# Performance work log

Measured on AMD Instinct MI355X. Metric: run time of the kernel, lower is better.

## Reference

```python
import jax, jax.numpy as jnp
import numpy as np
import math

B, W, D, H, K = 32, 512, 512, 8, 64
DH = D // H

def _rms(x, s, eps=1e-6):
    return x / jnp.sqrt(jnp.mean(x * x, axis=-1, keepdims=True) + eps) * s

def _l2n(x):
    return x / (jnp.linalg.norm(x, axis=-1, keepdims=True) + 1e-6)

def _rope(x, fc):
    b, t, h, d = x.shape
    xc = jax.lax.complex(x[..., 0::2], x[..., 1::2])
    xr = xc * fc
    return jnp.stack([xr.real, xr.imag], axis=-1).reshape(b, t, h, d)

def setup_inputs() -> dict:
    key = jax.random.key(0)
    ks = jax.random.split(key, 24)
    n = lambda i, s: jax.random.normal(ks[i], s, jnp.float32) * 0.02
    return {
        'x': jax.random.normal(ks[0], (B, W, D), jnp.float32),
        'epi_keys': _l2n(jax.random.normal(ks[1], (B, K, D), jnp.float32)),
        'epi_vals': jax.random.normal(ks[2], (B, K, D), jnp.float32),
        'epi_age': jax.random.uniform(ks[3], (B, K), jnp.float32, 0.0, 10.0),
        'epi_strength': jax.random.uniform(ks[4], (B, K), jnp.float32, 0.01, 1.0),
        'pos_idx': jnp.arange(W, dtype=jnp.int32),
        'rms1': jnp.ones((D,), jnp.float32), 'rms_kv': jnp.ones((D,), jnp.float32),
        'rms2': jnp.ones((D,), jnp.float32), 'rms_read': jnp.ones((D,), jnp.float32),
        'Wq': n(5, (D, D)), 'bq': jnp.zeros((D,), jnp.float32),
        'Wk': n(6, (D, D)), 'bk': jnp.zeros((D,), jnp.float32),
        'Wv': n(7, (D, D)), 'bv': jnp.zeros((D,), jnp.float32),
        'Wo': n(8, (D, D)), 'bo': jnp.zeros((D,), jnp.float32),
        'W1': n(9, (D, 8 * D)), 'W2': n(10, (4 * D, D)),
        'Wwk': n(11, (D, D)), 'bwk': jnp.zeros((D,), jnp.float32),
        'Wwv': n(12, (D, D)), 'bwv': jnp.zeros((D,), jnp.float32),
        'Wws': n(13, (D, 1)), 'bws': jnp.zeros((1,), jnp.float32),
        'Wg1': n(14, (D + 2, D)), 'bg1': jnp.zeros((D,), jnp.float32),
        'Wg2': n(15, (D, 1)), 'bg2': jnp.zeros((1,), jnp.float32),
    }

def _cell(x, epi_keys, epi_vals, epi_age, epi_strength, pos_idx,
          rms1, rms_kv, rms2, rms_read, Wq, bq, Wk, bk, Wv, bv, Wo, bo,
          W1, W2, Wwk, bwk, Wwv, bwv, Wws, bws, Wg1, bg1, Wg2, bg2):
    Bc, T, Dc = x.shape
    # RoPE freqs at absolute window positions (slice_freqs_cis)
    freqs = 1.0 / (10000.0 ** (jnp.arange(0, DH, 2, dtype=jnp.float32) / DH))  # (DH/2,)
    ang = pos_idx.astype(jnp.float32)[:, None] * freqs[None, :]               # (T, DH/2)
    fc = jax.lax.complex(jnp.cos(ang), jnp.sin(ang))[None, :, None, :]        # (1,T,1,DH/2)
    # --- windowed causal RoPE attention (TransformerBlock) ---
    nx, nkv = _rms(x, rms1), _rms(x, rms_kv)
    q = _rope((nx @ Wq + bq).reshape(Bc, T, H, DH), fc)
    k = _rope((nkv @ Wk + bk).reshape(Bc, T, H, DH), fc)
    v = (nkv @ Wv + bv).reshape(Bc, T, H, DH)
    att = jnp.einsum('bthd,bshd->bhts', q, k) / math.sqrt(DH)
    causal = jnp.tril(jnp.ones((T, T), bool))
    att = jnp.where(causal[None, None], att, -1e9)
    p = jax.nn.softmax(att, axis=-1)
    o = jnp.einsum('bhts,bshd->bthd', p, v).reshape(Bc, T, Dc)
    h1 = x + (o @ Wo + bo)
    gv = _rms(h1, rms2) @ W1
    g, val = jnp.split(gv, 2, axis=-1)
    h2 = h1 + (jax.nn.silu(g) * val) @ W2                                     # (B,T,D)
    # --- window summary query ---
    q_win = jnp.mean(h2, axis=1)                                              # (B,D)
    # --- EpisodicSlotReader ---
    qn = _l2n(q_win)
    kn = _l2n(epi_keys)
    sim_r = jnp.sum(kn * qn[:, None, :], axis=-1)                             # (B,K)
    logits = sim_r + 0.5 * jnp.log(jnp.clip(epi_strength, 0.001, 1e9)) - 0.02 * epi_age
    logits = logits + ((epi_strength > 0.001).astype(jnp.float32) - 1.0) * 1000.0
    w_read = jax.nn.softmax(logits, axis=-1)
    read = _rms(jnp.sum(w_read[:, :, None] * epi_vals, axis=1), rms_read)     # (B,D)
    # --- write projections ---
    write_key = q_win @ Wwk + bwk
    write_val = q_win @ Wwv + bwv
    ws = jnp.clip(jax.nn.sigmoid(q_win @ Wws + bws), 0.0, 1.0)                # (B,1)
    # --- EpisodicSlotWriter (ST top-1 competitive write) ---
    wk_n = _l2n(write_key)
    sim_w = jnp.sum(kn * wk_n[:, None, :], axis=-1)                           # (B,K)
    soft = jax.nn.softmax(sim_w * 50.0, axis=-1)
    hard = jax.nn.one_hot(jnp.argmax(soft, axis=-1), K, dtype=jnp.float32)
    write_w = jax.lax.stop_gradient(hard - soft) + soft
    eff = write_w * ws * 0.5                                                  # (B,K)
    re = eff[:, :, None]
    keys_new = _l2n((1.0 - re) * epi_keys + re * write_key[:, None, :])
    vals_new = (1.0 - re) * epi_vals + re * write_val[:, None, :]
    age_new = (epi_age + 1.0) * (1.0 - write_w)
    sn = epi_strength * 0.995
    sn = jnp.clip(sn + write_w * ws * (1.0 - sn), 0.001, 1.0)
    best_sim = jnp.max(sim_w, axis=-1)                                        # (B,)
    # --- MemoryRecallGate ---
    novelty = (1.0 - best_sim)[:, None]
    xg = jnp.concatenate([q_win, ws, novelty], axis=-1)                       # (B,D+2)
    gate = jax.nn.sigmoid(jax.nn.silu(xg @ Wg1 + bg1) @ Wg2 + bg2)            # (B,1)
    out = h2 + (gate * read)[:, None, :]
    return out, keys_new, vals_new, age_new, sn, gate

def reference(x, epi_keys, epi_vals, epi_age, epi_strength, pos_idx,
              rms1, rms_kv, rms2, rms_read, Wq, bq, Wk, bk, Wv, bv, Wo, bo,
              W1, W2, Wwk, bwk, Wwv, bwv, Wws, bws, Wg1, bg1, Wg2, bg2):
    return _cell(x, epi_keys, epi_vals, epi_age, epi_strength, pos_idx,
                 rms1, rms_kv, rms2, rms_read, Wq, bq, Wk, bk, Wv, bv, Wo, bo,
                 W1, W2, Wwk, bwk, Wwv, bwv, Wws, bws, Wg1, bg1, Wg2, bg2)
```

## Files before the change

### kernel.cpp

```cpp
#include <hip/hip_runtime.h>


#define DEVI __device__ __forceinline__
typedef unsigned short u16;
typedef unsigned int   u32;
typedef __bf16 v8bf __attribute__((ext_vector_type(8)));
typedef float  v4f  __attribute__((ext_vector_type(4)));

DEVI float bf2f(u16 u) { u32 v = ((u32)u) << 16; return __builtin_bit_cast(float, v); }
DEVI u16 f2bf(float f) {
  u32 x = __builtin_bit_cast(u32, f);
  u32 r = x + 0x7fffu + ((x >> 16) & 1u);
  return (u16)(r >> 16);
}
DEVI uint4 pack8(const float* f) {
  u32 a[4];
#pragma unroll
  for (int i = 0; i < 4; ++i)
    a[i] = (u32)f2bf(f[2*i]) | ((u32)f2bf(f[2*i+1]) << 16);
  uint4 v; v.x = a[0]; v.y = a[1]; v.z = a[2]; v.w = a[3]; return v;
}
DEVI void ld8f(const float* p, float* f) {
  float4 a = *(const float4*)p, b = *(const float4*)(p + 4);
  f[0]=a.x; f[1]=a.y; f[2]=a.z; f[3]=a.w; f[4]=b.x; f[5]=b.y; f[6]=b.z; f[7]=b.w;
}
DEVI void st8f(float* p, const float* f) {
  *(float4*)p       = make_float4(f[0], f[1], f[2], f[3]);
  *(float4*)(p + 4) = make_float4(f[4], f[5], f[6], f[7]);
}
DEVI v8bf ldfrag(const u16* p) { return __builtin_bit_cast(v8bf, *(const uint4*)p); }

DEVI u32 rot1(u32 w, float c, float s) {
  float e = bf2f((u16)(w & 0xffffu)), o = bf2f((u16)(w >> 16));
  float ne = e * c - o * s;
  float no = e * s + o * c;
  return (u32)f2bf(ne) | ((u32)f2bf(no) << 16);
}

DEVI void async16(const u16* g, u16* l) {
  __builtin_amdgcn_global_load_lds(
      (const __attribute__((address_space(1))) void*)g,
      (__attribute__((address_space(3))) void*)l, 16, 0, 0);
}

DEVI float wave_sum64(float v) {
  v += __shfl_xor(v, 1);  v += __shfl_xor(v, 2);  v += __shfl_xor(v, 4);
  v += __shfl_xor(v, 8);  v += __shfl_xor(v, 16); v += __shfl_xor(v, 32);
  return v;
}

__device__ float block_sum256(float v, float* sred) {
  v = wave_sum64(v);
  int w = threadIdx.x >> 6;
  __syncthreads();
  if ((threadIdx.x & 63) == 0) sred[w] = v;
  __syncthreads();
  return sred[0] + sred[1] + sred[2] + sred[3];
}

__global__ __launch_bounds__(256) void prep_k(
    const float* __restrict__ Wq, const float* __restrict__ Wk,
    const float* __restrict__ Wv, const float* __restrict__ Wo,
    const float* __restrict__ W1, const float* __restrict__ W2,
    const float* __restrict__ rms1, const float* __restrict__ rms_kv,
    const float* __restrict__ rms2, u16* __restrict__ WTqkv,
    u16* __restrict__ WTo, u16* __restrict__ WT1, u16* __restrict__ WT2,
    const float* __restrict__ bq, const float* __restrict__ bk,
    const float* __restrict__ bv, float* __restrict__ bias_qkv,
    const int* __restrict__ pos, float* __restrict__ tbl,
    float* __restrict__ qw_g, const float* __restrict__ x,
    u16* __restrict__ nrm) {
  int id = blockIdx.x;
  int tid = threadIdx.x;
  if (id >= 4230) {
    int w = tid >> 6, lane = tid & 63;
    size_t row = (size_t)(id - 4230) * 4 + w;
    float xf[8]; ld8f(x + row * 512 + lane * 8, xf);
    float ss = 0.f;
#pragma unroll
    for (int i = 0; i < 8; ++i) ss += xf[i] * xf[i];
    ss = wave_sum64(ss);
    float inv = rsqrtf(ss * (1.f / 512.f) + 1e-6f);
    float of[8];
#pragma unroll
    for (int i = 0; i < 8; ++i) of[i] = xf[i] * inv;
    *(uint4*)(nrm + row * 512 + lane * 8) = pack8(of);
    return;
  }
  if (id >= 4166) {
    qw_g[(id - 4166) * 256 + tid] = 0.f;
    return;
  }
  if (id >= 4102) {
    int idx = (id - 4102) * 256 + tid;
    int t = idx >> 5, f = idx & 31;
    float freq = exp2f(-0.41524101186f * (float)f);
    float ang = (float)pos[t] * freq;
    float sv, cv;
    sincosf(ang, &sv, &cv);
    tbl[t * 64 + f * 2]     = cv;
    tbl[t * 64 + f * 2 + 1] = sv;
    return;
  }
  if (id >= 4096) {
    int j = (id - 4096) * 256 + tid;
    bias_qkv[j] = j < 512 ? bq[j] : (j < 1024 ? bk[j - 512] : bv[j - 1024]);
    return;
  }
  const float* in; const float* scale; u16* outp; int R, C, bx, by;
  if (id < 256)       { in=Wq; scale=rms1;   outp=WTqkv;            R=512;  C=512;  int l=id;       bx=l&15;  by=l>>4; }
  else if (id < 512)  { in=Wk; scale=rms_kv; outp=WTqkv+512*512;    R=512;  C=512;  int l=id-256;   bx=l&15;  by=l>>4; }
  else if (id < 768)  { in=Wv; scale=rms_kv; outp=WTqkv+1024*512;   R=512;  C=512;  int l=id-512;   bx=l&15;  by=l>>4; }
  else if (id < 1024) { in=Wo; scale=nullptr;outp=WTo;              R=512;  C=512;  int l=id-768;   bx=l&15;  by=l>>4; }
  else if (id < 3072) { in=W1; scale=rms2;   outp=WT1;              R=512;  C=4096; int l=id-1024;  bx=l&127; by=l>>7; }
  else                { in=W2; scale=nullptr;outp=WT2;              R=2048; C=512;  int l=id-3072;  bx=l&15;  by=l>>4; }
  __shared__ u16 t[32][33];
  int c0 = bx * 32, r0 = by * 32;
  int lc = tid & 31, lr = tid >> 5;
  for (int rr = lr; rr < 32; rr += 8) {
    float v = in[(size_t)(r0 + rr) * C + c0 + lc];
    if (scale) v *= scale[r0 + rr];
    t[rr][lc] = f2bf(v);
  }
  __syncthreads();
  for (int rr = lr; rr < 32; rr += 8)
    outp[(size_t)(c0 + rr) * R + r0 + lc] = t[lc][rr];
}

__global__ __launch_bounds__(256) void rms_k(const float* __restrict__ x,
                                             u16* __restrict__ o1) {
  int w = threadIdx.x >> 6, lane = threadIdx.x & 63;
  size_t row = (size_t)blockIdx.x * 4 + w;
  float xf[8]; ld8f(x + row * 512 + lane * 8, xf);
  float ss = 0.f;
#pragma unroll
  for (int i = 0; i < 8; ++i) ss += xf[i] * xf[i];
  ss = wave_sum64(ss);
  float inv = rsqrtf(ss * (1.f / 512.f) + 1e-6f);
  float of[8];
#pragma unroll
  for (int i = 0; i < 8; ++i) of[i] = xf[i] * inv;
  *(uint4*)(o1 + row * 512 + lane * 8) = pack8(of);
}

__global__ __launch_bounds__(256) void gemm128_k(const u16* __restrict__ A,
                                                 const u16* __restrict__ BT,
                                                 const float* __restrict__ bias,
                                                 const float* __restrict__ resf,
                                                 u16* __restrict__ outb,
                                                 float* __restrict__ outf,
                                                 float* __restrict__ colsum,
                                                 int N, int Kd) {
  __shared__ u16 As[128 * 64];
  __shared__ u16 Bs[128 * 64];
  int tid = threadIdx.x;
  int w = tid >> 6, lane = tid & 63;
  int m = lane & 15, quad = lane >> 4;
  int wm = w >> 1, wn = w & 1;
  int bm = blockIdx.x, bn = blockIdx.y;
  v4f acc[4][4] = {};
  const int gswz = ((lane & 7) ^ (lane >> 3)) * 8;
  const u16* Ag = A + (size_t)(bm * 128 + w * 32 + (lane >> 3)) * Kd + gswz;
  const u16* Bg = BT + (size_t)(bn * 128 + w * 32 + (lane >> 3)) * Kd + gswz;
  u16* Al = &As[w * 32 * 64];
  u16* Bl = &Bs[w * 32 * 64];
  const int rsw = (m & 7) * 8;
  for (int k0 = 0; k0 < Kd; k0 += 64) {
#pragma unroll
    for (int it = 0; it < 4; ++it) {
      async16(Ag + (size_t)it * 8 * Kd + k0, Al + it * 8 * 64);
      async16(Bg + (size_t)it * 8 * Kd + k0, Bl + it * 8 * 64);
    }
    __syncthreads();
#pragma unroll
    for (int kk = 0; kk < 2; ++kk) {
      v8bf af[4], bfr[4];
#pragma unroll
      for (int i = 0; i < 4; ++i)
        af[i] = ldfrag(&As[(wm * 64 + i * 16 + m) * 64 +
                           ((kk * 32 + quad * 8) ^ rsw)]);
#pragma unroll
      for (int j = 0; j < 4; ++j)
        bfr[j] = ldfrag(&Bs[(wn * 64 + j * 16 + m) * 64 +
                            ((kk * 32 + quad * 8) ^ rsw)]);
#pragma unroll
      for (int i = 0; i < 4; ++i)
#pragma unroll
        for (int j = 0; j < 4; ++j)
          acc[i][j] = __builtin_amdgcn_mfma_f32_16x16x32_bf16(af[i], bfr[j],
                                                              acc[i][j], 0, 0, 0);
    }
    __syncthreads();
  }
  float csum[4] = {0.f, 0.f, 0.f, 0.f};
#pragma unroll
  for (int i = 0; i < 4; ++i) {
    int grow0 = bm * 128 + wm * 64 + i * 16 + quad * 4;
#pragma unroll
    for (int j = 0; j < 4; ++j) {
      int gcol = bn * 128 + wn * 64 + j * 16 + m;
      float bv = bias ? bias[gcol] : 0.f;
#pragma unroll
      for (int rr = 0; rr < 4; ++rr) {
        size_t idx = (size_t)(grow0 + rr) * N + gcol;
        float v = acc[i][j][rr] + bv;
        if (resf) v += resf[idx];
        if (outb) outb[idx] = f2bf(v);
        else      outf[idx] = v;
        if (colsum) csum[j] += v;
      }
    }
  }
  if (colsum) {
    float* cs = (float*)As;
    __syncthreads();
    if (tid < 128) cs[tid] = 0.f;
    __syncthreads();
    int lc = wn * 64 + m;
#pragma unroll
    for (int j = 0; j < 4; ++j) atomicAdd(&cs[lc + j * 16], csum[j]);
    __syncthreads();
    if (tid < 128) {
      int b = bm >> 2;
      atomicAdd(colsum + (size_t)b * 512 + bn * 128 + tid,
                cs[tid] * (1.f / 512.f));
    }
  }
}

__global__ __launch_bounds__(256) void mlp1_k(const u16* __restrict__ A,
                                              const u16* __restrict__ W1T,
                                              u16* __restrict__ out) {
  __shared__ u16 As[128 * 64];
  __shared__ u16 Bgs[64 * 64];
  __shared__ u16 Bvs[64 * 64];
  const int Kd = 512;
  int tid = threadIdx.x;
  int w = tid >> 6, lane = tid & 63;
  int m = lane & 15, quad = lane >> 4;
  int bm = blockIdx.x, bn = blockIdx.y;
  v4f accg[2][4] = {}, accv[2][4] = {};
  const int gswz = ((lane & 7) ^ (lane >> 3)) * 8;
  const u16* Ag  = A + (size_t)(bm * 128 + w * 32 + (lane >> 3)) * Kd + gswz;
  const u16* Bgp = W1T + (size_t)(bn * 64 + w * 16 + (lane >> 3)) * Kd + gswz;
  const u16* Bvp = W1T + (size_t)(2048 + bn * 64 + w * 16 + (lane >> 3)) * Kd + gswz;
  u16* Al  = &As[w * 32 * 64];
  u16* Bgl = &Bgs[w * 16 * 64];
  u16* Bvl = &Bvs[w * 16 * 64];
  const int rsw = (m & 7) * 8;
  for (int k0 = 0; k0 < Kd; k0 += 64) {
#pragma unroll
    for (int it = 0; it < 4; ++it)
      async16(Ag + (size_t)it * 8 * Kd + k0, Al + it * 8 * 64);
#pragma unroll
    for (int it = 0; it < 2; ++it) {
      async16(Bgp + (size_t)it * 8 * Kd + k0, Bgl + it * 8 * 64);
      async16(Bvp + (size_t)it * 8 * Kd + k0, Bvl + it * 8 * 64);
    }
    __syncthreads();
#pragma unroll
    for (int kk = 0; kk < 2; ++kk) {
      v8bf af[2], bg[4], bv[4];
#pragma unroll
      for (int i = 0; i < 2; ++i)
        af[i] = ldfrag(&As[(w * 32 + i * 16 + m) * 64 +
                           ((kk * 32 + quad * 8) ^ rsw)]);
#pragma unroll
      for (int j = 0; j < 4; ++j) {
        bg[j] = ldfrag(&Bgs[(j * 16 + m) * 64 + ((kk * 32 + quad * 8) ^ rsw)]);
        bv[j] = ldfrag(&Bvs[(j * 16 + m) * 64 + ((kk * 32 + quad * 8) ^ rsw)]);
      }
#pragma unroll
      for (int i = 0; i < 2; ++i)
#pragma unroll
        for (int j = 0; j < 4; ++j) {
          accg[i][j] = __builtin_amdgcn_mfma_f32_16x16x32_bf16(af[i], bg[j],
                                                               accg[i][j], 0, 0, 0);
          accv[i][j] = __builtin_amdgcn_mfma_f32_16x16x32_bf16(af[i], bv[j],
                                                               accv[i][j], 0, 0, 0);
        }
    }
    __syncthreads();
  }
#pragma unroll
  for (int i = 0; i < 2; ++i) {
    int grow0 = bm * 128 + w * 32 + i * 16 + quad * 4;
#pragma unroll
    for (int j = 0; j < 4; ++j) {
      int gcol = bn * 64 + j * 16 + m;
#pragma unroll
      for (int rr = 0; rr < 4; ++rr) {
        float g = accg[i][j][rr];
        float sv = g / (1.f + __expf(-g));
        out[(size_t)(grow0 + rr) * 2048 + gcol] = f2bf(sv * accv[i][j][rr]);
      }
    }
  }
}

__global__ __launch_bounds__(1024) void attn_k(const u16* __restrict__ qkv,
                                               const float* __restrict__ tbl,
                                               u16* __restrict__ og) {
  __shared__ u16 Ks[512 * 64];
  __shared__ u16 Vt[64 * 512];
  __shared__ u16 Ps[16][16 * 40];
  int tid = threadIdx.x;
  int w = tid >> 6, lane = tid & 63;
  int m = lane & 15, quad = lane >> 4;
  int bh = blockIdx.x;
  int b = bh >> 3, h = bh & 7;
  const size_t qbase = (size_t)b * 512 * 1536 + h * 64;
  const size_t obase = (size_t)b * 512 * 512 + h * 64;
  const u16* kbase = qkv + (size_t)b * 512 * 1536 + 512 + h * 64;
  const u16* vbase = kbase + 512;

  {
    int d8 = (tid & 7) * 8;
    for (int s = tid >> 3; s < 512; s += 128) {
      uint4 t4 = *(const uint4*)(kbase + (size_t)s * 1536 + d8);
      const float4* tp = (const float4*)(tbl + s * 64 + d8);
      float4 cs01 = tp[0], cs23 = tp[1];
      t4.x = rot1(t4.x, cs01.x, cs01.y);
      t4.y = rot1(t4.y, cs01.z, cs01.w);
      t4.z = rot1(t4.z, cs23.x, cs23.y);
      t4.w = rot1(t4.w, cs23.z, cs23.w);
      *(uint4*)&Ks[s * 64 + (d8 ^ ((s & 7) * 8))] = t4;
    }
  }
  {
    int d0 = (tid & 7) * 8;
    for (int s = tid >> 3; s < 512; s += 128) {
      uint4 v4 = *(const uint4*)(vbase + (size_t)s * 1536 + d0);
      const u16* vv = (const u16*)&v4;
#pragma unroll
      for (int j = 0; j < 8; ++j) {
        int d = d0 + j;
        Vt[d * 512 + (s ^ ((d & 7) * 8))] = vv[j];
      }
    }
  }
  __syncthreads();

  for (int rep = 0; rep < 2; ++rep) {
    int qt = rep == 0 ? w : 31 - w;
    int tb = qt * 16;
    const u16* qp = qkv + qbase + (size_t)(tb + m) * 1536;
    uint4 q0 = *(const uint4*)(qp + quad * 8);
    uint4 q1 = *(const uint4*)(qp + 32 + quad * 8);
    {
      const float* tq = tbl + (tb + m) * 64;
      float4 a = *(const float4*)(tq + quad * 8);
      float4 b4 = *(const float4*)(tq + quad * 8 + 4);
      q0.x = rot1(q0.x, a.x, a.y);   q0.y = rot1(q0.y, a.z, a.w);
      q0.z = rot1(q0.z, b4.x, b4.y); q0.w = rot1(q0.w, b4.z, b4.w);
      float4 c4 = *(const float4*)(tq + 32 + quad * 8);
      float4 d4 = *(const float4*)(tq + 36 + quad * 8);
      q1.x = rot1(q1.x, c4.x, c4.y); q1.y = rot1(q1.y, c4.z, c4.w);
      q1.z = rot1(q1.z, d4.x, d4.y); q1.w = rot1(q1.w, d4.z, d4.w);
    }
    v8bf aq0 = __builtin_bit_cast(v8bf, q0);
    v8bf aq1 = __builtin_bit_cast(v8bf, q1);
    v4f acc[4] = {};
    float mr[4], lr_[4];
#pragma unroll
    for (int rr = 0; rr < 4; ++rr) { mr[rr] = -1.0e30f; lr_[rr] = 0.f; }
    int swz = (m & 7) * 8;

    for (int st2 = 0; st2 <= qt; st2 += 2) {
      int srA = st2 * 16 + m;
      v8bf ka0 = ldfrag(&Ks[srA * 64 + ((quad * 8) ^ swz)]);
      v8bf ka1 = ldfrag(&Ks[srA * 64 + ((32 + quad * 8) ^ swz)]);
      v4f s4a = {};
      __builtin_amdgcn_s_setprio(1);
      s4a = __builtin_amdgcn_mfma_f32_16x16x32_bf16(aq0, ka0, s4a, 0, 0, 0);
      s4a = __builtin_amdgcn_mfma_f32_16x16x32_bf16(aq1, ka1, s4a, 0, 0, 0);
      __builtin_amdgcn_s_setprio(0);
      bool haveB = (st2 + 1 <= qt);
      v4f s4b = {};
      if (haveB) {
        int srB = srA + 16;
        v8bf kb0 = ldfrag(&Ks[srB * 64 + ((quad * 8) ^ swz)]);
        v8bf kb1 = ldfrag(&Ks[srB * 64 + ((32 + quad * 8) ^ swz)]);
        __builtin_amdgcn_s_setprio(1);
        s4b = __builtin_amdgcn_mfma_f32_16x16x32_bf16(aq0, kb0, s4b, 0, 0, 0);
        s4b = __builtin_amdgcn_mfma_f32_16x16x32_bf16(aq1, kb1, s4b, 0, 0, 0);
        __builtin_amdgcn_s_setprio(0);
      }
      float sca[4], scb[4];
#pragma unroll
      for (int rr = 0; rr < 4; ++rr) {
        int rowt = tb + quad * 4 + rr;
        sca[rr] = s4a[rr] * 0.125f;
        if (st2 == qt && st2 * 16 + m > rowt) sca[rr] = -1.0e9f;
        scb[rr] = haveB ? s4b[rr] * 0.125f : -1.0e30f;
        if (haveB && st2 + 1 == qt && (st2 + 1) * 16 + m > rowt) scb[rr] = -1.0e9f;
      }
      float pva[4], pvb[4], alpha[4];
#pragma unroll
      for (int rr = 0; rr < 4; ++rr) {
        float v = fmaxf(sca[rr], scb[rr]);
        v = fmaxf(v, __shfl_xor(v, 1));
        v = fmaxf(v, __shfl_xor(v, 2));
        v = fmaxf(v, __shfl_xor(v, 4));
        v = fmaxf(v, __shfl_xor(v, 8));
        float mn = fmaxf(mr[rr], v);
        alpha[rr] = __expf(mr[rr] - mn);
        pva[rr] = __expf(sca[rr] - mn);
        pvb[rr] = __expf(scb[rr] - mn);
        mr[rr] = mn;
      }
#pragma unroll
      for (int rr = 0; rr < 4; ++rr) {
        float s = pva[rr] + pvb[rr];
        s += __shfl_xor(s, 1); s += __shfl_xor(s, 2);
        s += __shfl_xor(s, 4); s += __shfl_xor(s, 8);
        lr_[rr] = lr_[rr] * alpha[rr] + s;
#pragma unroll
        for (int c = 0; c < 4; ++c) acc[c][rr] *= alpha[rr];
        Ps[w][(quad * 4 + rr) * 40 + m]      = f2bf(pva[rr]);
        Ps[w][(quad * 4 + rr) * 40 + 16 + m] = f2bf(pvb[rr]);
      }
      __asm__ volatile("" ::: "memory");
      v8bf pf = ldfrag(&Ps[w][m * 40 + quad * 8]);
      __builtin_amdgcn_s_setprio(1);
#pragma unroll
      for (int c = 0; c < 4; ++c) {
        int drow = c * 16 + m;
        v8bf vf = ldfrag(&Vt[drow * 512 +
                             ((st2 * 16 + quad * 8) ^ ((drow & 7) * 8))]);
        acc[c] = __builtin_amdgcn_mfma_f32_16x16x32_bf16(pf, vf, acc[c], 0, 0, 0);
      }
      __builtin_amdgcn_s_setprio(0);
    }
#pragma unroll
    for (int rr = 0; rr < 4; ++rr) {
      int t = tb + quad * 4 + rr;
      float inv = 1.f / lr_[rr];
      u16* op = og + obase + (size_t)t * 512;
#pragma unroll
      for (int c = 0; c < 4; ++c) op[c * 16 + m] = f2bf(acc[c][rr] * inv);
    }
  }
}

__global__ __launch_bounds__(256) void gemv_k(
    const float* __restrict__ qw_g, const float* __restrict__ Wwk,
    const float* __restrict__ bwk, const float* __restrict__ Wwv,
    const float* __restrict__ bwv, const float* __restrict__ Wg1,
    const float* __restrict__ bg1, const float* __restrict__ Wws,
    const float* __restrict__ bws, float* __restrict__ wkey_g,
    float* __restrict__ wval_g, float* __restrict__ abase_g,
    float* __restrict__ ws_g) {
  __shared__ float qs[512];
  __shared__ float prt[4][64];
  __shared__ float sred[8];
  int tid = threadIdx.x;
  int b = blockIdx.y, cg = blockIdx.x;
  qs[tid]       = qw_g[(size_t)b * 512 + tid];
  qs[tid + 256] = qw_g[(size_t)b * 512 + tid + 256];
  __syncthreads();
  if (cg == 24) {
    float p = qs[tid] * Wws[tid] + qs[tid + 256] * Wws[tid + 256];
    float tot = block_sum256(p, sred);
    if (tid == 0) {
      float wsv = 1.f / (1.f + __expf(-(tot + bws[0])));
      ws_g[b] = fminf(fmaxf(wsv, 0.f), 1.f);
    }
    return;
  }
  int sel = cg >> 3;
  int c0 = (cg & 7) * 64;
  const float* W = sel == 0 ? Wwk : (sel == 1 ? Wwv : Wg1);
  const float* bias = sel == 0 ? bwk : (sel == 1 ? bwv : bg1);
  float* dst = sel == 0 ? wkey_g : (sel == 1 ? wval_g : abase_g);
  int kg = tid >> 6, cl = tid & 63;
  const float* Wp = W + (size_t)(kg * 128) * 512 + c0 + cl;
  float acc = 0.f;
#pragma unroll 8
  for (int i = 0; i < 128; ++i) acc += qs[kg * 128 + i] * Wp[(size_t)i * 512];
  prt[kg][cl] = acc;
  __syncthreads();
  if (tid < 64)
    dst[(size_t)b * 512 + c0 + tid] =
        prt[0][tid] + prt[1][tid] + prt[2][tid] + prt[3][tid] + bias[c0 + tid];
}

__global__ __launch_bounds__(256) void epi2_k(
    const float* __restrict__ qw_g, const float* __restrict__ wkey_g,
    const float* __restrict__ wval_g, const float* __restrict__ abase_g,
    const float* __restrict__ ws_g, const float* __restrict__ keys,
    const float* __restrict__ vals, const float* __restrict__ age,
    const float* __restrict__ strength, const float* __restrict__ Wg1,
    const float* __restrict__ Wg2, const float* __restrict__ bg2,
    const float* __restrict__ rms_read, float* __restrict__ read_f,
    float* __restrict__ gate_f, float* __restrict__ keys_out,
    float* __restrict__ vals_out, float* __restrict__ age_out,
    float* __restrict__ sn_out, float* __restrict__ gate_out) {
  int b = blockIdx.x;
  int tid = threadIdx.x;
  int w = tid >> 6, lane = tid & 63;
  __shared__ float qs[512], wkl[512], wvl[512];
  __shared__ float knorm[64], sr[64], swv[64], wread[64];
  __shared__ float sred[8];
  __shared__ float scal[2];
  __shared__ int bestk;
  __shared__ float novs;

  qs[tid]        = qw_g[(size_t)b * 512 + tid];
  qs[tid + 256]  = qw_g[(size_t)b * 512 + tid + 256];
  wkl[tid]       = wkey_g[(size_t)b * 512 + tid];
  wkl[tid + 256] = wkey_g[(size_t)b * 512 + tid + 256];
  wvl[tid]       = wval_g[(size_t)b * 512 + tid];
  wvl[tid + 256] = wval_g[(size_t)b * 512 + tid + 256];
  __syncthreads();
  float ws_s = ws_g[b];
  float p = qs[tid] * qs[tid] + qs[tid + 256] * qs[tid + 256];
  float tot = block_sum256(p, sred);
  if (tid == 0) scal[0] = 1.f / (sqrtf(tot) + 1e-6f);
  p = wkl[tid] * wkl[tid] + wkl[tid + 256] * wkl[tid + 256];
  tot = block_sum256(p, sred);
  if (tid == 0) scal[1] = 1.f / (sqrtf(tot) + 1e-6f);
  __syncthreads();
  float qscale = scal[0], wscale = scal[1];
  for (int k = w; k < 64; k += 4) {
    float kf[8];
    ld8f(keys + ((size_t)b * 64 + k) * 512 + lane * 8, kf);
    float s2 = 0.f, sq = 0.f, sw = 0.f;
#pragma unroll
    for (int i = 0; i < 8; ++i) {
      s2 += kf[i] * kf[i];
      sq += kf[i] * qs[lane * 8 + i];
      sw += kf[i] * wkl[lane * 8 + i];
    }
    s2 = wave_sum64(s2);
    sq = wave_sum64(sq);
    sw = wave_sum64(sw);
    if (lane == 0) {
      float kn = sqrtf(s2) + 1e-6f;
      knorm[k] = kn;
      float st = strength[b * 64 + k];
      float ag = age[b * 64 + k];
      sr[k] = (sq * qscale) / kn + 0.5f * logf(fminf(fmaxf(st, 0.001f), 1e9f)) -
              0.02f * ag + ((st > 0.001f) ? 0.f : -1000.f);
      swv[k] = (sw * wscale) / kn;
    }
  }
  __syncthreads();
  if (w == 0) {
    float v = sr[lane];
    float mx = v;
    mx = fmaxf(mx, __shfl_xor(mx, 1));  mx = fmaxf(mx, __shfl_xor(mx, 2));
    mx = fmaxf(mx, __shfl_xor(mx, 4));  mx = fmaxf(mx, __shfl_xor(mx, 8));
    mx = fmaxf(mx, __shfl_xor(mx, 16)); mx = fmaxf(mx, __shfl_xor(mx, 32));
    float e = __expf(v - mx);
    float sm = wave_sum64(e);
    wread[lane] = e / sm;
  } else if (w == 1) {
    float v = swv[lane];
    int idx = lane;
#pragma unroll
    for (int mm = 1; mm < 64; mm <<= 1) {
      float ov = __shfl_xor(v, mm);
      int oi = __shfl_xor(idx, mm);
      if (ov > v || (ov == v && oi < idx)) { v = ov; idx = oi; }
    }
    if (lane == 0) { bestk = idx; novs = 1.f - v; }
  }
  __syncthreads();
  float rv0 = 0.f, rv1 = 0.f;
  for (int k = 0; k < 64; ++k) {
    float wr = wread[k];
    const float* vp = vals + ((size_t)b * 64 + k) * 512;
    rv0 += wr * vp[tid];
    rv1 += wr * vp[tid + 256];
  }
  p = rv0 * rv0 + rv1 * rv1;
  tot = block_sum256(p, sred);
  float rinv = rsqrtf(tot * (1.f / 512.f) + 1e-6f);
  read_f[(size_t)b * 512 + tid]       = rv0 * rinv * rms_read[tid];
  read_f[(size_t)b * 512 + tid + 256] = rv1 * rinv * rms_read[tid + 256];
  if (tid < 64) {
    int k = tid;
    float hard = (k == bestk) ? 1.f : 0.f;
    float ag = age[b * 64 + k];
    age_out[b * 64 + k] = (ag + 1.f) * (1.f - hard);
    float st = strength[b * 64 + k];
    float s0 = st * 0.995f;
    float snv = s0 + hard * ws_s * (1.f - s0);
    sn_out[b * 64 + k] = fminf(fmaxf(snv, 0.001f), 1.f);
  }
  for (int k = w; k < 64; k += 4) {
    float re = (k == bestk) ? ws_s * 0.5f : 0.f;
    float kf[8], vf[8];
    ld8f(keys + ((size_t)b * 64 + k) * 512 + lane * 8, kf);
    ld8f(vals + ((size_t)b * 64 + k) * 512 + lane * 8, vf);
    float u[8], ss = 0.f;
#pragma unroll
    for (int i = 0; i < 8; ++i) {
      u[i] = (1.f - re) * kf[i] + re * wkl[lane * 8 + i];
      ss += u[i] * u[i];
    }
    ss = wave_sum64(ss);
    float uinv = 1.f / (sqrtf(ss) + 1e-6f);
    float ko[8], vo[8];
#pragma unroll
    for (int i = 0; i < 8; ++i) {
      ko[i] = u[i] * uinv;
      vo[i] = (1.f - re) * vf[i] + re * wvl[lane * 8 + i];
    }
    st8f(keys_out + ((size_t)b * 64 + k) * 512 + lane * 8, ko);
    st8f(vals_out + ((size_t)b * 64 + k) * 512 + lane * 8, vo);
  }
  __syncthreads();
  float nov = novs;
  float a0 = abase_g[(size_t)b * 512 + tid] +
             ws_s * Wg1[(size_t)512 * 512 + tid] +
             nov * Wg1[(size_t)513 * 512 + tid];
  float a1 = abase_g[(size_t)b * 512 + tid + 256] +
             ws_s * Wg1[(size_t)512 * 512 + tid + 256] +
             nov * Wg1[(size_t)513 * 512 + tid + 256];
  float h0 = a0 / (1.f + __expf(-a0));
  float h1v = a1 / (1.f + __expf(-a1));
  float gp = h0 * Wg2[tid] + h1v * Wg2[tid + 256];
  tot = block_sum256(gp, sred);
  if (tid == 0) {
    float g = 1.f / (1.f + __expf(-(tot + bg2[0])));
    gate_f[b] = g;
    gate_out[b] = g;
  }
}

__global__ __launch_bounds__(256) void final_k(const float* __restrict__ h2,
                                               const float* __restrict__ read_f,
                                               const float* __restrict__ gate_f,
                                               float* __restrict__ outp) {
  size_t i2 = ((size_t)blockIdx.x * 256 + threadIdx.x) * 2;
  int b = (int)(i2 >> 18);
  int d = (int)(i2 & 511);
  float g = gate_f[b];
  float2 h = *(const float2*)(h2 + i2);
  outp[i2]     = h.x + g * read_f[b * 512 + d];
  outp[i2 + 1] = h.y + g * read_f[b * 512 + d + 1];
}

extern "C" void kernel_launch(void* const* d_in, const int* in_sizes, int n_in,
                              void* d_out, int out_size, void* d_ws,
                              size_t ws_size, hipStream_t stream) {
  const float* x        = (const float*)d_in[0];
  const float* epi_keys = (const float*)d_in[1];
  const float* epi_vals = (const float*)d_in[2];
  const float* epi_age  = (const float*)d_in[3];
  const float* epi_str  = (const float*)d_in[4];
  const int*   pos      = (const int*)d_in[5];
  const float* rms1     = (const float*)d_in[6];
  const float* rms_kv   = (const float*)d_in[7];
  const float* rms2     = (const float*)d_in[8];
  const float* rms_read = (const float*)d_in[9];
  const float* Wq = (const float*)d_in[10]; const float* bq = (const float*)d_in[11];
  const float* Wk = (const float*)d_in[12]; const float* bk = (const float*)d_in[13];
  const float* Wv = (const float*)d_in[14]; const float* bv = (const float*)d_in[15];
  const float* Wo = (const float*)d_in[16]; const float* bo = (const float*)d_in[17];
  const float* W1 = (const float*)d_in[18]; const float* W2 = (const float*)d_in[19];
  const float* Wwk = (const float*)d_in[20]; const float* bwk = (const float*)d_in[21];
  const float* Wwv = (const float*)d_in[22]; const float* bwv = (const float*)d_in[23];
  const float* Wws = (const float*)d_in[24]; const float* bws = (const float*)d_in[25];
  const float* Wg1 = (const float*)d_in[26]; const float* bg1 = (const float*)d_in[27];
  const float* Wg2 = (const float*)d_in[28]; const float* bg2 = (const float*)d_in[29];

  float* out      = (float*)d_out;
  float* out_main = out;
  float* out_keys = out + 8388608;
  float* out_vals = out + 9437184;
  float* out_age  = out + 10485760;
  float* out_sn   = out + 10487808;
  float* out_gate = out + 10489856;

  char* w8 = (char*)d_ws;
  size_t off = 0;
  auto alloc = [&](size_t bytes) {
    char* pp = w8 + off;
    off += (bytes + 255) & ~(size_t)255;
    return pp;
  };
  u16* WTqkv = (u16*)alloc((size_t)1536 * 512 * 2);
  u16* WTo   = (u16*)alloc(512 * 512 * 2);
  u16* WT1   = (u16*)alloc((size_t)4096 * 512 * 2);
  u16* WT2   = (u16*)alloc((size_t)512 * 2048 * 2);
  const size_t TB = (size_t)16384 * 512 * 2;
  u16* nrm  = (u16*)alloc(TB);
  u16* qkvb = (u16*)alloc(3 * TB);
  u16* ob   = (u16*)alloc(TB);
  u16* n2   = (u16*)alloc(TB);
  float* h1f = (float*)alloc((size_t)16384 * 512 * 4);
  u16*   gact = nrm;
  float* h2f  = (float*)ob;
  float* bias_qkv = (float*)alloc(1536 * 4);
  float* tbl      = (float*)alloc((size_t)512 * 64 * 4);
  float* qw_g     = (float*)alloc((size_t)32 * 512 * 4);
  float* wkey_g   = (float*)alloc((size_t)32 * 512 * 4);
  float* wval_g   = (float*)alloc((size_t)32 * 512 * 4);
  float* abase_g  = (float*)alloc((size_t)32 * 512 * 4);
  float* ws_g     = (float*)alloc(64 * 4);
  float* read_f   = (float*)alloc((size_t)32 * 512 * 4);
  float* gate_f   = (float*)alloc(64 * 4);

  prep_k<<<8326, 256, 0, stream>>>(Wq, Wk, Wv, Wo, W1, W2, rms1, rms_kv, rms2,
                                   WTqkv, WTo, WT1, WT2, bq, bk, bv, bias_qkv,
                                   pos, tbl, qw_g, x, nrm);
  gemm128_k<<<dim3(128, 12), 256, 0, stream>>>(nrm, WTqkv, bias_qkv, nullptr,
                                               qkvb, nullptr, nullptr, 1536, 512);
  attn_k<<<256, 1024, 0, stream>>>(qkvb, tbl, ob);
  gemm128_k<<<dim3(128, 4), 256, 0, stream>>>(ob, WTo, bo, x,
                                              nullptr, h1f, nullptr, 512, 512);
  rms_k<<<4096, 256, 0, stream>>>(h1f, n2);
  mlp1_k<<<dim3(128, 32), 256, 0, stream>>>(n2, WT1, gact);
  gemm128_k<<<dim3(128, 4), 256, 0, stream>>>(gact, WT2, nullptr, h1f,
                                              nullptr, h2f, qw_g, 512, 2048);
  gemv_k<<<dim3(25, 32), 256, 0, stream>>>(qw_g, Wwk, bwk, Wwv, bwv, Wg1, bg1,
                                           Wws, bws, wkey_g, wval_g, abase_g, ws_g);
  epi2_k<<<32, 256, 0, stream>>>(qw_g, wkey_g, wval_g, abase_g, ws_g, epi_keys,
                                 epi_vals, epi_age, epi_str, Wg1, Wg2, bg2,
                                 rms_read, read_f, gate_f, out_keys, out_vals,
                                 out_age, out_sn, out_gate);
  final_k<<<16384, 256, 0, stream>>>(h2f, read_f, gate_f, out_main);
}
```

Measured before the change: 498.8 us.

## Fuse second RMSNorm into Wo GEMM epilogue and MLP1 output scaling

Removes the standalone rms_k pass over h1. The Wo GEMM epilogue now also writes a bf16 copy of the unnormalized h1 and atomically accumulates per-row sums of squares. mlp1_k applies the rsqrt row scale to both GEMM outputs, which is valid because the normalization is a per-row scalar. This saves one full read of h1 and the write of n2, at the cost of atomics, an extra zeroing pass in prep_k, and bf16 rounding applied before normalization instead of after.

After: 506.8 us. About the same (+1.6%).

```diff
diff --git a/kernel.cpp b/kernel.cpp
--- a/kernel.cpp
+++ b/kernel.cpp
@@ -68,13 +68,13 @@
     const float* __restrict__ bq, const float* __restrict__ bk,
     const float* __restrict__ bv, float* __restrict__ bias_qkv,
     const int* __restrict__ pos, float* __restrict__ tbl,
-    float* __restrict__ qw_g, const float* __restrict__ x,
-    u16* __restrict__ nrm) {
+    float* __restrict__ qw_g, float* __restrict__ rssq,
+    const float* __restrict__ x, u16* __restrict__ nrm) {
   int id = blockIdx.x;
   int tid = threadIdx.x;
-  if (id >= 4230) {
+  if (id >= 4294) {
     int w = tid >> 6, lane = tid & 63;
-    size_t row = (size_t)(id - 4230) * 4 + w;
+    size_t row = (size_t)(id - 4294) * 4 + w;
     float xf[8]; ld8f(x + row * 512 + lane * 8, xf);
     float ss = 0.f;
 #pragma unroll
@@ -85,6 +85,10 @@
 #pragma unroll
     for (int i = 0; i < 8; ++i) of[i] = xf[i] * inv;
     *(uint4*)(nrm + row * 512 + lane * 8) = pack8(of);
+    return;
+  }
+  if (id >= 4230) {
+    rssq[(id - 4230) * 256 + tid] = 0.f;
     return;
   }
   if (id >= 4166) {
@@ -127,28 +131,14 @@
     outp[(size_t)(c0 + rr) * R + r0 + lc] = t[lc][rr];
 }
 
-__global__ __launch_bounds__(256) void rms_k(const float* __restrict__ x,
-                                             u16* __restrict__ o1) {
-  int w = threadIdx.x >> 6, lane = threadIdx.x & 63;
-  size_t row = (size_t)blockIdx.x * 4 + w;
-  float xf[8]; ld8f(x + row * 512 + lane * 8, xf);
-  float ss = 0.f;
-#pragma unroll
-  for (int i = 0; i < 8; ++i) ss += xf[i] * xf[i];
-  ss = wave_sum64(ss);
-  float inv = rsqrtf(ss * (1.f / 512.f) + 1e-6f);
-  float of[8];
-#pragma unroll
-  for (int i = 0; i < 8; ++i) of[i] = xf[i] * inv;
-  *(uint4*)(o1 + row * 512 + lane * 8) = pack8(of);
-}
-
 __global__ __launch_bounds__(256) void gemm128_k(const u16* __restrict__ A,
                                                  const u16* __restrict__ BT,
                                                  const float* __restrict__ bias,
                                                  const float* __restrict__ resf,
                                                  u16* __restrict__ outb,
                                                  float* __restrict__ outf,
+                                                 u16* __restrict__ outb2,
+                                                 float* __restrict__ rowssq,
                                                  float* __restrict__ colsum,
                                                  int N, int Kd) {
   __shared__ u16 As[128 * 64];
@@ -196,6 +186,7 @@
 #pragma unroll
   for (int i = 0; i < 4; ++i) {
     int grow0 = bm * 128 + wm * 64 + i * 16 + quad * 4;
+    float rq[4] = {0.f, 0.f, 0.f, 0.f};
 #pragma unroll
     for (int j = 0; j < 4; ++j) {
       int gcol = bn * 128 + wn * 64 + j * 16 + m;
@@ -207,7 +198,18 @@
         if (resf) v += resf[idx];
         if (outb) outb[idx] = f2bf(v);
         else      outf[idx] = v;
+        if (outb2) outb2[idx] = f2bf(v);
         if (colsum) csum[j] += v;
+        if (rowssq) rq[rr] += v * v;
+      }
+    }
+    if (rowssq) {
+#pragma unroll
+      for (int rr = 0; rr < 4; ++rr) {
+        float s = rq[rr];
+        s += __shfl_xor(s, 1); s += __shfl_xor(s, 2);
+        s += __shfl_xor(s, 4); s += __shfl_xor(s, 8);
+        if (m == 0) atomicAdd(rowssq + grow0 + rr, s);
       }
     }
   }
@@ -230,6 +232,7 @@
 
 __global__ __launch_bounds__(256) void mlp1_k(const u16* __restrict__ A,
                                               const u16* __restrict__ W1T,
+                                              const float* __restrict__ rssq,
                                               u16* __restrict__ out) {
   __shared__ u16 As[128 * 64];
   __shared__ u16 Bgs[64 * 64];
@@ -285,14 +288,19 @@
 #pragma unroll
   for (int i = 0; i < 2; ++i) {
     int grow0 = bm * 128 + w * 32 + i * 16 + quad * 4;
+    float inv[4];
+#pragma unroll
+    for (int rr = 0; rr < 4; ++rr)
+      inv[rr] = rsqrtf(rssq[grow0 + rr] * (1.f / 512.f) + 1e-6f);
 #pragma unroll
     for (int j = 0; j < 4; ++j) {
       int gcol = bn * 64 + j * 16 + m;
 #pragma unroll
       for (int rr = 0; rr < 4; ++rr) {
-        float g = accg[i][j][rr];
+        float g = accg[i][j][rr] * inv[rr];
         float sv = g / (1.f + __expf(-g));
-        out[(size_t)(grow0 + rr) * 2048 + gcol] = f2bf(sv * accv[i][j][rr]);
+        out[(size_t)(grow0 + rr) * 2048 + gcol] =
+            f2bf(sv * (accv[i][j][rr] * inv[rr]));
       }
     }
   }
@@ -690,13 +698,14 @@
   u16* nrm  = (u16*)alloc(TB);
   u16* qkvb = (u16*)alloc(3 * TB);
   u16* ob   = (u16*)alloc(TB);
-  u16* n2   = (u16*)alloc(TB);
+  u16* h1b  = (u16*)alloc(TB);
   float* h1f = (float*)alloc((size_t)16384 * 512 * 4);
   u16*   gact = nrm;
   float* h2f  = (float*)ob;
   float* bias_qkv = (float*)alloc(1536 * 4);
   float* tbl      = (float*)alloc((size_t)512 * 64 * 4);
   float* qw_g     = (float*)alloc((size_t)32 * 512 * 4);
+  float* rssq     = (float*)alloc((size_t)16384 * 4);
   float* wkey_g   = (float*)alloc((size_t)32 * 512 * 4);
   float* wval_g   = (float*)alloc((size_t)32 * 512 * 4);
   float* abase_g  = (float*)alloc((size_t)32 * 512 * 4);
@@ -704,18 +713,20 @@
   float* read_f   = (float*)alloc((size_t)32 * 512 * 4);
   float* gate_f   = (float*)alloc(64 * 4);
 
-  prep_k<<<8326, 256, 0, stream>>>(Wq, Wk, Wv, Wo, W1, W2, rms1, rms_kv, rms2,
+  prep_k<<<8390, 256, 0, stream>>>(Wq, Wk, Wv, Wo, W1, W2, rms1, rms_kv, rms2,
                                    WTqkv, WTo, WT1, WT2, bq, bk, bv, bias_qkv,
-                                   pos, tbl, qw_g, x, nrm);
+                                   pos, tbl, qw_g, rssq, x, nrm);
   gemm128_k<<<dim3(128, 12), 256, 0, stream>>>(nrm, WTqkv, bias_qkv, nullptr,
-                                               qkvb, nullptr, nullptr, 1536, 512);
+                                               qkvb, nullptr, nullptr, nullptr,
+                                               nullptr, 1536, 512);
   attn_k<<<256, 1024, 0, stream>>>(qkvb, tbl, ob);
   gemm128_k<<<dim3(128, 4), 256, 0, stream>>>(ob, WTo, bo, x,
-                                              nullptr, h1f, nullptr, 512, 512);
-  rms_k<<<4096, 256, 0, stream>>>(h1f, n2);
-  mlp1_k<<<dim3(128, 32), 256, 0, stream>>>(n2, WT1, gact);
+                                              nullptr, h1f, h1b, rssq,
+                                              nullptr, 512, 512);
+  mlp1_k<<<dim3(128, 32), 256, 0, stream>>>(h1b, WT1, rssq, gact);
   gemm128_k<<<dim3(128, 4), 256, 0, stream>>>(gact, WT2, nullptr, h1f,
-                                              nullptr, h2f, qw_g, 512, 2048);
+                                              nullptr, h2f, nullptr, nullptr,
+                                              qw_g, 512, 2048);
   gemv_k<<<dim3(25, 32), 256, 0, stream>>>(qw_g, Wwk, bwk, Wwv, bwv, Wg1, bg1,
                                            Wws, bws, wkey_g, wval_g, abase_g, ws_g);
   epi2_k<<<32, 256, 0, stream>>>(qw_g, wkey_g, wval_g, abase_g, ws_g, epi_keys,
```
